# Performance work log

Hardware: AMD Instinct MI355X
Metric: run time of the kernel (lower is better)

## Reference

```python
import jax, jax.numpy as jnp
import numpy as np

B, S, ENC, HID = 2, 2048, 2048, 2048
HQ, HKV, D = 8, 4, 256
SOFTCAP = 50.0
SCALING = float(256) ** -0.5  # query_pre_attn_scalar ** -0.5
EPS = 1e-6
NEG = -1e9  # finite stand-in for -inf in additive masks


def _rms_norm(x, w, eps=EPS):
    # GemmaRMSNorm: fp32 compute, scale by (1 + weight)
    xf = x.astype(jnp.float32)
    n = xf * jax.lax.rsqrt(jnp.mean(xf * xf, axis=-1, keepdims=True) + eps)
    return (n * (1.0 + w.astype(jnp.float32))).astype(x.dtype)


def _rotate_half(x):
    x1, x2 = jnp.split(x, 2, axis=-1)
    return jnp.concatenate([-x2, x1], axis=-1)


def _apply_rope(q, k, cos, sin):
    # q,k: [B, H, S, D]; cos,sin: [1, S, D] -> unsqueeze head dim
    c, s = cos[:, None, :, :], sin[:, None, :, :]
    return q * c + _rotate_half(q) * s, k * c + _rotate_half(k) * s


def setup_inputs() -> dict:
    key = jax.random.key(0)
    ks = jax.random.split(key, 8)
    hidden_states = jax.random.normal(ks[0], (B, S, HID), jnp.float32)
    encoder_hidden_states = jax.random.normal(ks[1], (B, ENC, HID), jnp.float32)
    # RoPE tables (base 10000)
    pos = jnp.arange(S, dtype=jnp.float32)
    inv_freq = 1.0 / (10000.0 ** (jnp.arange(0, D, 2, dtype=jnp.float32) / D))
    freqs = pos[:, None] * inv_freq[None, :]                 # [S, D/2]
    emb = jnp.concatenate([freqs, freqs], axis=-1)           # [S, D]
    cos = jnp.cos(emb)[None]                                 # [1, S, D]
    sin = jnp.sin(emb)[None]
    # merged additive mask: causal over self part, fully visible cross part
    causal = jnp.where(jnp.arange(S)[:, None] >= jnp.arange(S)[None, :], 0.0, NEG)
    mask = jnp.concatenate([causal, jnp.zeros((S, ENC), jnp.float32)], axis=-1)
    merged_attention_mask = mask[None, None].astype(jnp.float32)  # [1,1,S,S+ENC]
    w = 0.02
    Wq = jax.random.normal(ks[2], (HQ * D, HID), jnp.float32) * w
    Wk = jax.random.normal(ks[3], (HKV * D, HID), jnp.float32) * w
    Wv = jax.random.normal(ks[4], (HKV * D, HID), jnp.float32) * w
    Wo = jax.random.normal(ks[5], (HID, HQ * D), jnp.float32) * w
    q_norm_w = jnp.zeros((D,), jnp.float32)
    k_norm_w = jnp.zeros((D,), jnp.float32)
    return dict(hidden_states=hidden_states, encoder_hidden_states=encoder_hidden_states,
                cos=cos, sin=sin, merged_attention_mask=merged_attention_mask,
                Wq=Wq, Wk=Wk, Wv=Wv, Wo=Wo, q_norm_w=q_norm_w, k_norm_w=k_norm_w)


def reference(hidden_states, encoder_hidden_states, cos, sin, merged_attention_mask,
              Wq, Wk, Wv, Wo, q_norm_w, k_norm_w):
    b, s, _ = hidden_states.shape
    enc = encoder_hidden_states.shape[1]
    n_rep = HQ // HKV
    # projections
    q = hidden_states @ Wq.T                                 # [B,S,HQ*D]
    k_self = hidden_states @ Wk.T
    v_self = hidden_states @ Wv.T
    k_cross = encoder_hidden_states @ Wk.T
    v_cross = encoder_hidden_states @ Wv.T
    q = q.reshape(b, s, HQ, D).transpose(0, 2, 1, 3)         # [B,HQ,S,D]
    k_self = k_self.reshape(b, s, HKV, D).transpose(0, 2, 1, 3)
    v_self = v_self.reshape(b, s, HKV, D).transpose(0, 2, 1, 3)
    k_cross = k_cross.reshape(b, enc, HKV, D).transpose(0, 2, 1, 3)
    v_cross = v_cross.reshape(b, enc, HKV, D).transpose(0, 2, 1, 3)
    # QK RMSNorm + RoPE (RoPE only on self q/k)
    q = _rms_norm(q, q_norm_w)
    k_self = _rms_norm(k_self, k_norm_w)
    k_cross = _rms_norm(k_cross, k_norm_w)
    q, k_self = _apply_rope(q, k_self, cos, sin)
    # merged KV + GQA repeat
    k = jnp.concatenate([k_self, k_cross], axis=2)           # [B,HKV,S+ENC,D]
    v = jnp.concatenate([v_self, v_cross], axis=2)
    k = jnp.repeat(k, n_rep, axis=1)                         # [B,HQ,S+ENC,D]
    v = jnp.repeat(v, n_rep, axis=1)
    # eager softcapped attention
    scores = jnp.einsum('bhqd,bhkd->bhqk', q, k) * SCALING
    scores = SOFTCAP * jnp.tanh(scores / SOFTCAP)
    scores = scores + merged_attention_mask
    probs = jax.nn.softmax(scores, axis=-1)
    attn = jnp.einsum('bhqk,bhkd->bhqd', probs, v)           # [B,HQ,S,D]
    attn = attn.transpose(0, 2, 1, 3).reshape(b, s, HQ * D)
    return attn @ Wo.T
```

## Files before the change

### kernel.cpp

```cpp
#include <hip/hip_runtime.h>
#include <cstdint>

typedef __attribute__((ext_vector_type(8))) short bf16x8;
typedef __attribute__((ext_vector_type(4))) float f32x4;

#define B_ 2
#define S_ 2048
#define ENC_ 2048
#define HID_ 2048
#define HQ_ 8
#define HKV_ 4
#define D_ 256
#define L_ 4096

__device__ __forceinline__ short f2bf(float f) {
  uint32_t u = __builtin_bit_cast(uint32_t, f);
  u = (u + 0x7fffu + ((u >> 16) & 1u)) >> 16;
  return (short)u;
}
__device__ __forceinline__ float bf2f(short s) {
  uint32_t u = ((uint32_t)(uint16_t)s) << 16;
  return __builtin_bit_cast(float, u);
}
__device__ __forceinline__ uint32_t cvtpk(float lo, float hi) {
  uint32_t r;
  asm("v_cvt_pk_bf16_f32 %0, %1, %2" : "=v"(r) : "v"(lo), "v"(hi));
  return r;
}

__device__ __forceinline__ void llds16(const void* g, void* s) {
  __builtin_amdgcn_global_load_lds(
      (const __attribute__((address_space(1))) void*)(__builtin_bit_cast(uintptr_t, g)),
      (__attribute__((address_space(3))) void*)(uint32_t)(__builtin_bit_cast(uintptr_t, s)),
      16, 0, 0);
}

__device__ __forceinline__ void wg_barrier() {
  asm volatile("" ::: "memory");
  __builtin_amdgcn_s_barrier();
  asm volatile("" ::: "memory");
}

__global__ __launch_bounds__(256) void cvt_f32_bf16(const float* __restrict__ in,
                                                    short* __restrict__ out, int n) {
  int i = (blockIdx.x * 256 + threadIdx.x) * 4;
  if (i >= n) return;
  float4 v = *(const float4*)(in + i);
  short4 r;
  r.x = f2bf(v.x); r.y = f2bf(v.y); r.z = f2bf(v.z); r.w = f2bf(v.w);
  *(short4*)(out + i) = r;
}

template <int BM, int WM, int BF16OUT>
__global__ __launch_bounds__(512, 2)
void gemm_ring(const short* __restrict__ A, const short* __restrict__ Bw,
               void* __restrict__ Cout, int M, int N, int K) {
  constexpr int BN = 256;
  constexpr int LA = BM * 8 / 512;
  constexpr int LB = BN * 8 / 512;
  constexpr int LTOT = LA + LB;
  __shared__ __align__(16) short As[2][BM * 64];
  __shared__ __align__(16) short Bs[2][BN * 64];
  const int t = threadIdx.x;
  const int w = t >> 6, l = t & 63;
  const int lr = l & 15, lq = l >> 4, x7 = lr & 7;

  int nbx = N >> 8;
  int bid = blockIdx.x;
  int cpx = gridDim.x >> 3;
  int wg = (bid & 7) * cpx + (bid >> 3);
  int by = wg / nbx, bx = wg - (wg / nbx) * nbx;
  const int bm = by * BM, bn = bx * BN;
  const int wm = (w & 1) * WM, wn = (w >> 1) * 64;

  uint32_t goffA[LA], soffA[LA], goffB[LB], soffB[LB];
#pragma unroll
  for (int i = 0; i < LA; i++) {
    int slot = i * 512 + t;
    int row = slot >> 3, cp = slot & 7;
    goffA[i] = (uint32_t)((bm + row) * K + ((cp ^ (row & 7)) * 8));
    soffA[i] = (uint32_t)(slot * 8);
  }
#pragma unroll
  for (int i = 0; i < LB; i++) {
    int slot = i * 512 + t;
    int row = slot >> 3, cp = slot & 7;
    goffB[i] = (uint32_t)((bn + row) * K + ((cp ^ (row & 7)) * 8));
    soffB[i] = (uint32_t)(slot * 8);
  }

  auto stage = [&](int bufi, int k0) {
#pragma unroll
    for (int i = 0; i < LA; i++) llds16(A + (size_t)goffA[i] + k0, &As[bufi][soffA[i]]);
#pragma unroll
    for (int i = 0; i < LB; i++) llds16(Bw + (size_t)goffB[i] + k0, &Bs[bufi][soffB[i]]);
  };

  f32x4 acc[WM / 16][4];
#pragma unroll
  for (int mi = 0; mi < WM / 16; mi++)
#pragma unroll
    for (int ni = 0; ni < 4; ni++) acc[mi][ni] = f32x4{0.f, 0.f, 0.f, 0.f};

  const int NT = K >> 6;
  stage(0, 0);
  for (int tt = 0; tt < NT; tt++) {
    if (tt + 1 < NT) {
      stage((tt + 1) & 1, (tt + 1) << 6);
      if (LTOT == 8)
        asm volatile("s_waitcnt vmcnt(8)" ::: "memory");
      else
        asm volatile("s_waitcnt vmcnt(6)" ::: "memory");
    } else {
      asm volatile("s_waitcnt vmcnt(0)" ::: "memory");
    }
    wg_barrier();
    const char* Ab = (const char*)&As[tt & 1][0];
    const char* Bb = (const char*)&Bs[tt & 1][0];
#pragma unroll
    for (int ks = 0; ks < 2; ks++) {
      const int cof = ((4 * ks + lq) ^ x7) * 16;
      bf16x8 bfrag[4];
#pragma unroll
      for (int ni = 0; ni < 4; ni++)
        bfrag[ni] = *(const bf16x8*)(Bb + (wn + 16 * ni + lr) * 128 + cof);
#pragma unroll
      for (int mi = 0; mi < WM / 16; mi++) {
        bf16x8 af = *(const bf16x8*)(Ab + (wm + 16 * mi + lr) * 128 + cof);
#pragma unroll
        for (int ni = 0; ni < 4; ni++)
          acc[mi][ni] = __builtin_amdgcn_mfma_f32_16x16x32_bf16(af, bfrag[ni], acc[mi][ni], 0, 0, 0);
      }
    }
    wg_barrier();
  }

#pragma unroll
  for (int mi = 0; mi < WM / 16; mi++)
#pragma unroll
    for (int ni = 0; ni < 4; ni++)
#pragma unroll
      for (int r = 0; r < 4; r++) {
        int row = bm + wm + 16 * mi + lq * 4 + r;
        int col = bn + wn + 16 * ni + lr;
        float v = acc[mi][ni][r];
        if (BF16OUT)
          ((short*)Cout)[(size_t)row * N + col] = f2bf(v);
        else
          ((float*)Cout)[(size_t)row * N + col] = v;
      }
}

__global__ __launch_bounds__(256)
void norm_rope(const short* __restrict__ src, int src_ld, int col0, int H,
               short* __restrict__ dst, int dstL, int pos_off, int do_rope, int kswz,
               const float* __restrict__ wn, const float* __restrict__ cosp,
               const float* __restrict__ sinp) {
  __shared__ float sh[256];
  __shared__ float red[4];
  int bid = blockIdx.x;
  int s = bid & (S_ - 1);
  int h = (bid >> 11) % H;
  int b = (bid >> 11) / H;
  int d = threadIdx.x;
  int w = d >> 6, l = d & 63;
  float x = bf2f(src[(size_t)(b * S_ + s) * src_ld + col0 + h * D_ + d]);
  float ss = x * x;
#pragma unroll
  for (int off = 32; off; off >>= 1) ss += __shfl_xor(ss, off, 64);
  if (l == 0) red[w] = ss;
  __syncthreads();
  float tot = red[0] + red[1] + red[2] + red[3];
  float y = x * rsqrtf(tot * (1.0f / D_) + 1e-6f) * (1.0f + wn[d]);
  float outv = y;
  if (do_rope) {
    sh[d] = y;
    __syncthreads();
    float c = cosp[s * D_ + d];
    float sn = sinp[s * D_ + d];
    outv = (d < 128) ? (y * c - sh[d + 128] * sn) : (y * c + sh[d - 128] * sn);
  }
  int dd = d;
  if (kswz) dd = (((d >> 3) ^ (s & 7)) << 3) | (d & 7);
  dst[((size_t)(b * H + h) * dstL + pos_off + s) * D_ + dd] = f2bf(outv);
}

__global__ __launch_bounds__(256)
void v_transpose(const short* __restrict__ qkv_self, const short* __restrict__ kv_cross,
                 short* __restrict__ Vt) {
  __shared__ __align__(16) short tile[64][72];
  int bid = blockIdx.x;
  int dt = bid & 3;
  int lt = (bid >> 2) & 63;
  int h = (bid >> 8) & 3;
  int b = bid >> 10;
  int t = threadIdx.x;
  int rl = t >> 2;
  int cc = (t & 3) * 16;
  int l = lt * 64 + rl;
  const short* src;
  if (lt < 32)
    src = qkv_self + (size_t)(b * S_ + l) * 4096 + 3072 + h * D_ + dt * 64 + cc;
  else
    src = kv_cross + (size_t)(b * ENC_ + (l - S_)) * 2048 + 1024 + h * D_ + dt * 64 + cc;
  *(bf16x8*)&tile[rl][cc] = *(const bf16x8*)src;
  *(bf16x8*)&tile[rl][cc + 8] = *(const bf16x8*)(src + 8);
  __syncthreads();
  int dl = t >> 2;
  int lc = (t & 3) * 16;
  bf16x8 v0, v1;
#pragma unroll
  for (int j = 0; j < 8; j++) {
    v0[j] = tile[lc + j][dl];
    v1[j] = tile[lc + 8 + j][dl];
  }
  int d = dt * 64 + dl;
  int e3 = (dl >> 1) & 3;
  int c0 = 2 * (t & 3);
  int c1 = c0 + 1;
  int p0 = (c0 & 4) | ((c0 ^ e3) & 3);
  int p1 = (c1 & 4) | ((c1 ^ e3) & 3);
  short* rowp = Vt + ((size_t)(b * HKV_ + h) * D_ + d) * (size_t)L_ + lt * 64;
  *(bf16x8*)(rowp + p0 * 8) = v0;
  *(bf16x8*)(rowp + p1 * 8) = v1;
}

__global__ __launch_bounds__(256, 2)
void flash_attn(const short* __restrict__ Q, const short* __restrict__ K,
                const short* __restrict__ Vt, short* __restrict__ part0,
                short* __restrict__ part1, short* __restrict__ part2,
                short* __restrict__ part3, float* __restrict__ lsum) {
  __shared__ __align__(16) short Ks[2][32 * 256];
  __shared__ __align__(16) short Vs[2][256 * 32];
  __shared__ __align__(16) short Ps[4][2][16 * 40];
  int t = threadIdx.x, w = t >> 6, l = t & 63;
  int lr = l & 15, lq = l >> 4, x7 = lr & 7, vx = (lr >> 1) & 3;
  int bid = blockIdx.x;
  int pair = bid >> 6;
  int p = (bid >> 4) & 3;
  int bh = bid & 15;
  int b = bh >> 3, h = bh & 7, hk = h >> 1;
  short* op = (p == 0) ? part0 : (p == 1) ? part1 : (p == 2) ? part2 : part3;

  const short* Kbase = K + (size_t)(b * HKV_ + hk) * L_ * D_;
  const short* Vbase = Vt + (size_t)(b * HKV_ + hk) * (size_t)D_ * L_;

  uint32_t kofs[8];
#pragma unroll
  for (int kf = 0; kf < 8; kf++)
    kofs[kf] = (uint32_t)(lr * 512 + (((4 * kf + lq) ^ x7) * 16));
  const uint32_t vof = (uint32_t)(lr * 64 + ((lq ^ vx) * 16));

  const short* kg_lane = Kbase + (8 * w + (l >> 5)) * 256 + (l & 31) * 8;
  const short* vg_lane = Vbase + (size_t)(64 * w + (l >> 2)) * (size_t)L_ + (l & 3) * 8;
  short* ks_lane = &Ks[0][8 * w * 256 + l * 8];
  short* vs_lane = &Vs[0][64 * w * 32 + l * 8];

  auto stage = [&](int bufi, int k0) {
    const short* kg = kg_lane + (size_t)k0 * 256;
    short* ks = ks_lane + bufi * (32 * 256);
#pragma unroll
    for (int i = 0; i < 4; i++) llds16(kg + i * 512, ks + i * 512);
    const short* vg = vg_lane + k0;
    short* vs = vs_lane + bufi * (256 * 32);
#pragma unroll
    for (int i = 0; i < 4; i++) llds16(vg + (size_t)(16 * i) * L_, vs + i * 512);
  };

  int gi = p;
  const int lenA = 2 * pair + 34;

  for (int phase = 0; phase < 2; ++phase) {
    int qt = phase ? (15 - pair) : pair;
    int q0 = qt * 128;
    int nself = 2 * qt + 2;
    int base = phase ? lenA : 0;
    int lim = base + nself + 32;
    int qg0 = q0 + 32 * w + lr;
    int qg1 = qg0 + 16;

    bf16x8 qf0[8], qf1[8];
    {
      const short* qb0 = Q + ((size_t)(b * HQ_ + h) * S_ + qg0) * D_ + lq * 8;
      const short* qb1 = qb0 + (size_t)16 * D_;
#pragma unroll
      for (int kf = 0; kf < 8; kf++) {
        qf0[kf] = *(const bf16x8*)(qb0 + kf * 32);
        qf1[kf] = *(const bf16x8*)(qb1 + kf * 32);
      }
    }
    f32x4 o0[16], o1[16];
#pragma unroll
    for (int i = 0; i < 16; i++) {
      o0[i] = f32x4{0.f, 0.f, 0.f, 0.f};
      o1[i] = f32x4{0.f, 0.f, 0.f, 0.f};
    }
    float lacc0 = 0.f, lacc1 = 0.f;

    int gcur = gi, u = 0, buf = 0;
    {
      int local = gcur - base;
      int j = (local < nself) ? local : (local - nself + 32);
      stage(0, j * 64);
    }

    while (true) {
      int gn = gcur, un = u + 1;
      if (un == 2) { un = 0; gn = gcur + 4; }
      bool hn = (gn < lim);
      if (hn) {
        int localn = gn - base;
        int jn = (localn < nself) ? localn : (localn - nself + 32);
        stage(buf ^ 1, jn * 64 + 32 * un);
        asm volatile("s_waitcnt vmcnt(8)" ::: "memory");
      } else {
        asm volatile("s_waitcnt vmcnt(0)" ::: "memory");
      }
      wg_barrier();

      int local = gcur - base;
      int j = (local < nself) ? local : (local - nself + 32);
      int k0 = j * 64 + 32 * u;
      bool diag = (local >= nself - 2) && (local < nself);
      const char* KsB = (const char*)&Ks[buf][0];
      const char* VsB = (const char*)&Vs[buf][0];

      f32x4 sc[2][2];
#pragma unroll
      for (int nt = 0; nt < 2; nt++) {
        sc[nt][0] = f32x4{0.f, 0.f, 0.f, 0.f};
        sc[nt][1] = f32x4{0.f, 0.f, 0.f, 0.f};
      }
      __builtin_amdgcn_s_setprio(1);
#pragma unroll
      for (int kf = 0; kf < 8; kf++) {
#pragma unroll
        for (int nt = 0; nt < 2; nt++) {
          bf16x8 a = *(const bf16x8*)(KsB + kofs[kf] + nt * 8192);
          sc[nt][0] = __builtin_amdgcn_mfma_f32_16x16x32_bf16(a, qf0[kf], sc[nt][0], 0, 0, 0);
          sc[nt][1] = __builtin_amdgcn_mfma_f32_16x16x32_bf16(a, qf1[kf], sc[nt][1], 0, 0, 0);
        }
      }
      __builtin_amdgcn_s_setprio(0);

      f32x4 pe[2][2];
#pragma unroll
      for (int nt = 0; nt < 2; nt++)
#pragma unroll
        for (int qh = 0; qh < 2; qh++)
#pragma unroll
          for (int r = 0; r < 4; r++) {
            float s = sc[nt][qh][r];
            float t2 = s * s * 1.5625e-6f;
            float hh = fmaf(t2, -0.0033730157f, 0.0083333338f);
            hh = fmaf(t2, hh, -0.020833334f);
            hh = fmaf(t2, hh, 0.0625f);
            pe[nt][qh][r] = __expf(s * hh);
          }
      if (diag) {
        int kb = k0 + 4 * lq;
#pragma unroll
        for (int nt = 0; nt < 2; nt++)
#pragma unroll
          for (int r = 0; r < 4; r++) {
            if (kb + nt * 16 + r > qg0) pe[nt][0][r] = 0.f;
            if (kb + nt * 16 + r > qg1) pe[nt][1][r] = 0.f;
          }
      }
      lacc0 += (pe[0][0][0] + pe[0][0][1]) + (pe[0][0][2] + pe[0][0][3]) +
               (pe[1][0][0] + pe[1][0][1]) + (pe[1][0][2] + pe[1][0][3]);
      lacc1 += (pe[0][1][0] + pe[0][1][1]) + (pe[0][1][2] + pe[0][1][3]) +
               (pe[1][1][0] + pe[1][1][1]) + (pe[1][1][2] + pe[1][1][3]);
#pragma unroll
      for (int nt = 0; nt < 2; nt++) {
        *(uint2*)&Ps[w][0][lr * 40 + nt * 16 + lq * 4] =
            uint2{cvtpk(pe[nt][0][0], pe[nt][0][1]), cvtpk(pe[nt][0][2], pe[nt][0][3])};
        *(uint2*)&Ps[w][1][lr * 40 + nt * 16 + lq * 4] =
            uint2{cvtpk(pe[nt][1][0], pe[nt][1][1]), cvtpk(pe[nt][1][2], pe[nt][1][3])};
      }

      bf16x8 pb0 = *(const bf16x8*)&Ps[w][0][lr * 40 + lq * 8];
      bf16x8 pb1 = *(const bf16x8*)&Ps[w][1][lr * 40 + lq * 8];
      __builtin_amdgcn_s_setprio(1);
#pragma unroll
      for (int dt = 0; dt < 16; dt++) {
        bf16x8 va = *(const bf16x8*)(VsB + vof + dt * 1024);
        o0[dt] = __builtin_amdgcn_mfma_f32_16x16x32_bf16(va, pb0, o0[dt], 0, 0, 0);
        o1[dt] = __builtin_amdgcn_mfma_f32_16x16x32_bf16(va, pb1, o1[dt], 0, 0, 0);
      }
      __builtin_amdgcn_s_setprio(0);

      wg_barrier();
      if (!hn) break;
      gcur = gn; u = un; buf ^= 1;
    }
    gi = gcur + 4;

    size_t orow0 = ((size_t)b * S_ + qg0) * (HQ_ * D_) + h * D_;
    size_t orow1 = orow0 + (size_t)16 * (HQ_ * D_);
#pragma unroll
    for (int dt = 0; dt < 16; dt++) {
      *(uint2*)(op + orow0 + dt * 16 + 4 * lq) =
          uint2{cvtpk(o0[dt][0], o0[dt][1]), cvtpk(o0[dt][2], o0[dt][3])};
      *(uint2*)(op + orow1 + dt * 16 + 4 * lq) =
          uint2{cvtpk(o1[dt][0], o1[dt][1]), cvtpk(o1[dt][2], o1[dt][3])};
    }
    float lrow0 = lacc0, lrow1 = lacc1;
    lrow0 += __shfl_xor(lrow0, 16, 64);
    lrow0 += __shfl_xor(lrow0, 32, 64);
    lrow1 += __shfl_xor(lrow1, 16, 64);
    lrow1 += __shfl_xor(lrow1, 32, 64);
    if (lq == 0) {
      size_t lb = (((size_t)p * B_ + b) * HQ_ + h) * S_;
      lsum[lb + qg0] = lrow0;
      lsum[lb + qg1] = lrow1;
    }
  }
}

__global__ __launch_bounds__(256)
void combine4(const short* __restrict__ p0, const short* __restrict__ p1,
              const short* __restrict__ p2, const short* __restrict__ p3,
              const float* __restrict__ lsum, short* __restrict__ out) {
  int tid = blockIdx.x * 256 + threadIdx.x;
  size_t flat = (size_t)tid * 4;
  int h = ((int)(flat >> 8)) & 7;
  int s = ((int)(flat >> 11)) & 2047;
  int b = (int)(flat >> 22);
  size_t sbase = ((size_t)b * HQ_ + h) * S_ + s;
  const size_t SP = (size_t)B_ * HQ_ * S_;
  float inv = 1.0f / (lsum[sbase] + lsum[SP + sbase] + lsum[2 * SP + sbase] +
                      lsum[3 * SP + sbase]);
  short4 a = *(const short4*)(p0 + flat);
  short4 c = *(const short4*)(p1 + flat);
  short4 d = *(const short4*)(p2 + flat);
  short4 e = *(const short4*)(p3 + flat);
  short4 r;
  r.x = f2bf((bf2f(a.x) + bf2f(c.x) + bf2f(d.x) + bf2f(e.x)) * inv);
  r.y = f2bf((bf2f(a.y) + bf2f(c.y) + bf2f(d.y) + bf2f(e.y)) * inv);
  r.z = f2bf((bf2f(a.z) + bf2f(c.z) + bf2f(d.z) + bf2f(e.z)) * inv);
  r.w = f2bf((bf2f(a.w) + bf2f(c.w) + bf2f(d.w) + bf2f(e.w)) * inv);
  *(short4*)(out + flat) = r;
}

extern "C" void kernel_launch(void* const* d_in, const int* in_sizes, int n_in, void* d_out,
                              int out_size, void* d_ws, size_t ws_size, hipStream_t stream) {
  (void)in_sizes; (void)n_in; (void)out_size; (void)ws_size;
  const float* hidden = (const float*)d_in[0];
  const float* encoder = (const float*)d_in[1];
  const float* cosp = (const float*)d_in[2];
  const float* sinp = (const float*)d_in[3];
  const float* Wq = (const float*)d_in[5];
  const float* Wk = (const float*)d_in[6];
  const float* Wv = (const float*)d_in[7];
  const float* Wo = (const float*)d_in[8];
  const float* qnw = (const float*)d_in[9];
  const float* knw = (const float*)d_in[10];

  short* ws = (short*)d_ws;
  short* hs_bf = ws;
  short* enc_bf = ws + 8388608;
  short* wqkv_bf = ws + 16777216;
  short* wo_bf = ws + 25165824;
  short* qkv_self = ws + 29360128;
  short* kv_cross = ws + 46137344;
  short* Kb = ws + 54525952;
  short* Vtb = ws + 62914560;
  short* attn_b = hs_bf;
  short* Qb = enc_bf;
  short* part0 = qkv_self;
  short* part1 = qkv_self + 8388608;
  short* part2 = kv_cross;
  short* part3 = wqkv_bf;
  float* lsum = (float*)d_out;

  cvt_f32_bf16<<<8192, 256, 0, stream>>>(hidden, hs_bf, 8388608);
  cvt_f32_bf16<<<8192, 256, 0, stream>>>(encoder, enc_bf, 8388608);
  cvt_f32_bf16<<<4096, 256, 0, stream>>>(Wq, wqkv_bf, 4194304);
  cvt_f32_bf16<<<2048, 256, 0, stream>>>(Wk, wqkv_bf + 4194304, 2097152);
  cvt_f32_bf16<<<2048, 256, 0, stream>>>(Wv, wqkv_bf + 6291456, 2097152);
  cvt_f32_bf16<<<4096, 256, 0, stream>>>(Wo, wo_bf, 4194304);

  gemm_ring<256, 128, 1><<<256, 512, 0, stream>>>(hs_bf, wqkv_bf, qkv_self, 4096, 4096, 2048);
  gemm_ring<128, 64, 1><<<256, 512, 0, stream>>>(enc_bf, wqkv_bf + (size_t)2048 * 2048,
                                                 kv_cross, 4096, 2048, 2048);

  norm_rope<<<32768, 256, 0, stream>>>(qkv_self, 4096, 0, 8, Qb, 2048, 0, 1, 0, qnw, cosp, sinp);
  norm_rope<<<16384, 256, 0, stream>>>(qkv_self, 4096, 2048, 4, Kb, 4096, 0, 1, 1, knw, cosp, sinp);
  norm_rope<<<16384, 256, 0, stream>>>(kv_cross, 2048, 0, 4, Kb, 4096, 2048, 0, 1, knw, cosp, sinp);

  v_transpose<<<2048, 256, 0, stream>>>(qkv_self, kv_cross, Vtb);

  flash_attn<<<512, 256, 0, stream>>>(Qb, Kb, Vtb, part0, part1, part2, part3, lsum);
  combine4<<<16384, 256, 0, stream>>>(part0, part1, part2, part3, lsum, attn_b);

  gemm_ring<128, 64, 0><<<256, 512, 0, stream>>>(attn_b, wo_bf, d_out, 4096, 2048, 2048);
}
```

Measured before the change: 533.0 us.

## Merge conversion launches, vectorize norm_rope per-wave, use raw exp2 in softcap

Replaces six f32->bf16 conversion launches with one kernel that dispatches on block index. norm_rope now handles one row per wavefront with 4 elements per lane: rotate_half pairs come from a lane shuffle, so the LDS traffic and block barriers are gone and loads and stores are vectorized. In the attention inner loop the softcap polynomial coefficients are pre-scaled by log2(e) so that a raw v_exp_f32 replaces __expf. This drops a multiply per score, but the hand-rescaled constants could cost a little precision.

```diff
diff --git a/kernel.cpp b/kernel.cpp
--- a/kernel.cpp
+++ b/kernel.cpp
@@ -27,6 +27,11 @@
   asm("v_cvt_pk_bf16_f32 %0, %1, %2" : "=v"(r) : "v"(lo), "v"(hi));
   return r;
 }
+__device__ __forceinline__ float exp2_fast(float x) {
+  float r;
+  asm("v_exp_f32 %0, %1" : "=v"(r) : "v"(x));
+  return r;
+}
 
 __device__ __forceinline__ void llds16(const void* g, void* s) {
   __builtin_amdgcn_global_load_lds(
@@ -41,10 +46,24 @@
   asm volatile("" ::: "memory");
 }
 
-__global__ __launch_bounds__(256) void cvt_f32_bf16(const float* __restrict__ in,
-                                                    short* __restrict__ out, int n) {
-  int i = (blockIdx.x * 256 + threadIdx.x) * 4;
-  if (i >= n) return;
+__global__ __launch_bounds__(256)
+void cvt_all(const float* __restrict__ hid, const float* __restrict__ enc,
+             const float* __restrict__ wq, const float* __restrict__ wk,
+             const float* __restrict__ wv, const float* __restrict__ wo,
+             short* __restrict__ o_hid, short* __restrict__ o_enc,
+             short* __restrict__ o_wq, short* __restrict__ o_wk,
+             short* __restrict__ o_wv, short* __restrict__ o_wo) {
+  int bid = blockIdx.x;
+  const float* in;
+  short* out;
+  int off;
+  if (bid < 8192) { in = hid; out = o_hid; off = bid; }
+  else if (bid < 16384) { in = enc; out = o_enc; off = bid - 8192; }
+  else if (bid < 20480) { in = wq; out = o_wq; off = bid - 16384; }
+  else if (bid < 22528) { in = wk; out = o_wk; off = bid - 20480; }
+  else if (bid < 24576) { in = wv; out = o_wv; off = bid - 22528; }
+  else { in = wo; out = o_wo; off = bid - 24576; }
+  int i = (off * 256 + threadIdx.x) * 4;
   float4 v = *(const float4*)(in + i);
   short4 r;
   r.x = f2bf(v.x); r.y = f2bf(v.y); r.z = f2bf(v.z); r.w = f2bf(v.w);
@@ -156,33 +175,44 @@
                short* __restrict__ dst, int dstL, int pos_off, int do_rope, int kswz,
                const float* __restrict__ wn, const float* __restrict__ cosp,
                const float* __restrict__ sinp) {
-  __shared__ float sh[256];
-  __shared__ float red[4];
-  int bid = blockIdx.x;
-  int s = bid & (S_ - 1);
-  int h = (bid >> 11) % H;
-  int b = (bid >> 11) / H;
-  int d = threadIdx.x;
-  int w = d >> 6, l = d & 63;
-  float x = bf2f(src[(size_t)(b * S_ + s) * src_ld + col0 + h * D_ + d]);
-  float ss = x * x;
+  int wid = threadIdx.x >> 6;
+  int l = threadIdx.x & 63;
+  int row = blockIdx.x * 4 + wid;
+  int s = row & (S_ - 1);
+  int h = (row >> 11) % H;
+  int b = (row >> 11) / H;
+  int d0 = l * 4;
+  const short* sp = src + (size_t)(b * S_ + s) * src_ld + col0 + h * D_ + d0;
+  short4 xi = *(const short4*)sp;
+  float x0 = bf2f(xi.x), x1 = bf2f(xi.y), x2 = bf2f(xi.z), x3 = bf2f(xi.w);
+  float ss = (x0 * x0 + x1 * x1) + (x2 * x2 + x3 * x3);
 #pragma unroll
   for (int off = 32; off; off >>= 1) ss += __shfl_xor(ss, off, 64);
-  if (l == 0) red[w] = ss;
-  __syncthreads();
-  float tot = red[0] + red[1] + red[2] + red[3];
-  float y = x * rsqrtf(tot * (1.0f / D_) + 1e-6f) * (1.0f + wn[d]);
-  float outv = y;
+  float rn = rsqrtf(ss * (1.0f / D_) + 1e-6f);
+  float4 wv = *(const float4*)(wn + d0);
+  float y0 = x0 * rn * (1.0f + wv.x);
+  float y1 = x1 * rn * (1.0f + wv.y);
+  float y2 = x2 * rn * (1.0f + wv.z);
+  float y3 = x3 * rn * (1.0f + wv.w);
+  float o0 = y0, o1 = y1, o2 = y2, o3 = y3;
   if (do_rope) {
-    sh[d] = y;
-    __syncthreads();
-    float c = cosp[s * D_ + d];
-    float sn = sinp[s * D_ + d];
-    outv = (d < 128) ? (y * c - sh[d + 128] * sn) : (y * c + sh[d - 128] * sn);
+    float4 cv = *(const float4*)(cosp + s * D_ + d0);
+    float4 sv = *(const float4*)(sinp + s * D_ + d0);
+    float p0 = __shfl_xor(y0, 32, 64);
+    float p1 = __shfl_xor(y1, 32, 64);
+    float p2 = __shfl_xor(y2, 32, 64);
+    float p3 = __shfl_xor(y3, 32, 64);
+    float sgn = (l < 32) ? -1.f : 1.f;
+    o0 = fmaf(sgn * p0, sv.x, y0 * cv.x);
+    o1 = fmaf(sgn * p1, sv.y, y1 * cv.y);
+    o2 = fmaf(sgn * p2, sv.z, y2 * cv.z);
+    o3 = fmaf(sgn * p3, sv.w, y3 * cv.w);
   }
-  int dd = d;
-  if (kswz) dd = (((d >> 3) ^ (s & 7)) << 3) | (d & 7);
-  dst[((size_t)(b * H + h) * dstL + pos_off + s) * D_ + dd] = f2bf(outv);
+  int dd0 = d0;
+  if (kswz) dd0 = ((((d0 >> 3) ^ (s & 7)) << 3) | (d0 & 7));
+  short4 r;
+  r.x = f2bf(o0); r.y = f2bf(o1); r.z = f2bf(o2); r.w = f2bf(o3);
+  *(short4*)(dst + ((size_t)(b * H + h) * dstL + pos_off + s) * D_ + dd0) = r;
 }
 
 __global__ __launch_bounds__(256)
@@ -352,10 +382,10 @@
           for (int r = 0; r < 4; r++) {
             float s = sc[nt][qh][r];
             float t2 = s * s * 1.5625e-6f;
-            float hh = fmaf(t2, -0.0033730157f, 0.0083333338f);
-            hh = fmaf(t2, hh, -0.020833334f);
-            hh = fmaf(t2, hh, 0.0625f);
-            pe[nt][qh][r] = __expf(s * hh);
+            float hh = fmaf(t2, -0.0048662440f, 0.0120224587f);
+            hh = fmaf(t2, hh, -0.0300561468f);
+            hh = fmaf(t2, hh, 0.0901684401f);
+            pe[nt][qh][r] = exp2_fast(s * hh);
           }
       if (diag) {
         int kb = k0 + 4 * lq;
@@ -474,20 +504,16 @@
   short* part3 = wqkv_bf;
   float* lsum = (float*)d_out;
 
-  cvt_f32_bf16<<<8192, 256, 0, stream>>>(hidden, hs_bf, 8388608);
-  cvt_f32_bf16<<<8192, 256, 0, stream>>>(encoder, enc_bf, 8388608);
-  cvt_f32_bf16<<<4096, 256, 0, stream>>>(Wq, wqkv_bf, 4194304);
-  cvt_f32_bf16<<<2048, 256, 0, stream>>>(Wk, wqkv_bf + 4194304, 2097152);
-  cvt_f32_bf16<<<2048, 256, 0, stream>>>(Wv, wqkv_bf + 6291456, 2097152);
-  cvt_f32_bf16<<<4096, 256, 0, stream>>>(Wo, wo_bf, 4194304);
+  cvt_all<<<28672, 256, 0, stream>>>(hidden, encoder, Wq, Wk, Wv, Wo, hs_bf, enc_bf,
+                                     wqkv_bf, wqkv_bf + 4194304, wqkv_bf + 6291456, wo_bf);
 
   gemm_ring<256, 128, 1><<<256, 512, 0, stream>>>(hs_bf, wqkv_bf, qkv_self, 4096, 4096, 2048);
   gemm_ring<128, 64, 1><<<256, 512, 0, stream>>>(enc_bf, wqkv_bf + (size_t)2048 * 2048,
                                                  kv_cross, 4096, 2048, 2048);
 
-  norm_rope<<<32768, 256, 0, stream>>>(qkv_self, 4096, 0, 8, Qb, 2048, 0, 1, 0, qnw, cosp, sinp);
-  norm_rope<<<16384, 256, 0, stream>>>(qkv_self, 4096, 2048, 4, Kb, 4096, 0, 1, 1, knw, cosp, sinp);
-  norm_rope<<<16384, 256, 0, stream>>>(kv_cross, 2048, 0, 4, Kb, 4096, 2048, 0, 1, knw, cosp, sinp);
+  norm_rope<<<8192, 256, 0, stream>>>(qkv_self, 4096, 0, 8, Qb, 2048, 0, 1, 0, qnw, cosp, sinp);
+  norm_rope<<<4096, 256, 0, stream>>>(qkv_self, 4096, 2048, 4, Kb, 4096, 0, 1, 1, knw, cosp, sinp);
+  norm_rope<<<4096, 256, 0, stream>>>(kv_cross, 2048, 0, 4, Kb, 4096, 2048, 0, 1, knw, cosp, sinp);
 
   v_transpose<<<2048, 256, 0, stream>>>(qkv_self, kv_cross, Vtb);
 
```

Result: faster. 491.1 us (-7.9%).
